# Performance work log

Hardware: AMD Instinct MI355X
Metric: run time of the kernel (lower is better)

Reference implementation:

```python
import jax, jax.numpy as jnp
import numpy as np

# Faithful translation of NeuralAggregation.forward (bias=False path):
#   proj = features @ W
#   out[n] = elementwise max over {0} union {a * proj[n] : a in adjacency[n]}
# Because proj[n] is fixed while a ranges over scalars,
#   max_k (a_k * proj[n,d]) == max(amax_n * proj[n,d], amin_n * proj[n,d])
# where amax_n / amin_n are the per-node max/min neighbor values. This avoids
# materializing the [N, deg, D] intermediate and is mathematically identical.

N_NODES = 100000
DEG = 32
DIM = 256


def setup_inputs() -> dict:
    key = jax.random.key(0)
    k1, k2, k3 = jax.random.split(key, 3)
    features = jax.random.normal(k1, (N_NODES, DIM), dtype=jnp.float32)
    adjacency = jax.random.uniform(k2, (N_NODES, DEG), dtype=jnp.float32)
    W = jax.random.normal(k3, (DIM, DIM), dtype=jnp.float32) * (1.0 / np.sqrt(DIM)).astype(np.float32)
    return {"features": features, "adjacency": adjacency, "W": W}


def reference(features, adjacency, W):
    proj = features @ W  # [N, D]
    amax = jnp.max(adjacency, axis=1, keepdims=True)  # [N, 1]
    amin = jnp.min(adjacency, axis=1, keepdims=True)  # [N, 1]
    agg = jnp.maximum(amax * proj, amin * proj)       # max over neighbors, elementwise
    return jnp.maximum(agg, 0.0)                      # torch.zeros init of `returning`
```

## Files before the change

kernel.cpp:

```cpp
#include <hip/hip_runtime.h>

#define N_NODES 100000
#define DEG 32
#define DIM 256

typedef _Float16 f16x8 __attribute__((ext_vector_type(8)));
typedef float f32x4 __attribute__((ext_vector_type(4)));

__global__ void wprep_kernel(const float* __restrict__ W, _Float16* __restrict__ Wswz) {
    int tid = blockIdx.x * blockDim.x + threadIdx.x;
    int l = tid & 63;
    int frag = tid >> 6;
    int kt = frag >> 4;
    int nt = frag & 15;
    int col = nt * 16 + (l & 15);
    int kbase = kt * 32 + ((l >> 4) << 2);
    f16x8 v;
#pragma unroll
    for (int j = 0; j < 8; ++j) {
        int k = kbase + (j & 3) + ((j >> 2) << 4);
        v[j] = (_Float16)W[(size_t)k * DIM + col];
    }
    *reinterpret_cast<f16x8*>(Wswz + (size_t)tid * 8) = v;
}

__device__ __forceinline__ f16x8 cvt_a(float4 lo, float4 hi) {
    f16x8 af;
    af[0] = (_Float16)lo.x; af[1] = (_Float16)lo.y;
    af[2] = (_Float16)lo.z; af[3] = (_Float16)lo.w;
    af[4] = (_Float16)hi.x; af[5] = (_Float16)hi.y;
    af[6] = (_Float16)hi.z; af[7] = (_Float16)hi.w;
    return af;
}

__launch_bounds__(256, 4)
__global__ void agg_kernel(const float* __restrict__ F, const float* __restrict__ Adj,
                           const _Float16* __restrict__ Wswz, float* __restrict__ out) {
    __shared__ _Float16 sB[32 * 64 * 8];

    const int bx = blockIdx.x;
    const int m0 = bx * 64;
    const int t  = threadIdx.x;
    const int wv = t >> 6;
    const int l  = t & 63;
    const int lg = l >> 4;
    const int ll = l & 15;

#pragma unroll
    for (int i = 0; i < 8; ++i) {
        int c = wv * 8 + i;
        int kt = c >> 2, np = c & 3;
        int srcfrag = kt * 16 + np;
        f16x8 v = *reinterpret_cast<const f16x8*>(Wswz + ((size_t)srcfrag * 64 + l) * 8);
        *reinterpret_cast<f16x8*>(&sB[((size_t)c * 64 + l) * 8]) = v;
    }

    const int rrow = t >> 2;
    const int q    = t & 3;
    int radj = m0 + rrow;
    radj = radj < N_NODES ? radj : (N_NODES - 1);
    const float4* ap = reinterpret_cast<const float4*>(Adj + (size_t)radj * DEG) + q * 2;
    float4 ad0 = ap[0], ad1 = ap[1];

    int rowA = m0 + wv * 16 + ll;
    rowA = rowA < N_NODES ? rowA : (N_NODES - 1);
    const float4* Af4 = reinterpret_cast<const float4*>(F + (size_t)rowA * DIM) + lg;
    float4 plo[8], phi[8];
#pragma unroll
    for (int kt = 0; kt < 8; ++kt) { plo[kt] = Af4[kt * 8]; phi[kt] = Af4[kt * 8 + 4]; }

    float mx = fmaxf(fmaxf(ad0.x, ad0.y), fmaxf(ad0.z, ad0.w));
    mx = fmaxf(mx, fmaxf(fmaxf(ad1.x, ad1.y), fmaxf(ad1.z, ad1.w)));
    float mn = fminf(fminf(ad0.x, ad0.y), fminf(ad0.z, ad0.w));
    mn = fminf(mn, fminf(fminf(ad1.x, ad1.y), fminf(ad1.z, ad1.w)));
    mx = fmaxf(mx, __shfl_xor(mx, 1)); mn = fminf(mn, __shfl_xor(mn, 1));
    mx = fmaxf(mx, __shfl_xor(mx, 2)); mn = fminf(mn, __shfl_xor(mn, 2));
    float amaxr[4], aminr[4];
#pragma unroll
    for (int r = 0; r < 4; ++r) {
        amaxr[r] = __shfl(mx, 16 * lg + 4 * r);
        aminr[r] = __shfl(mn, 16 * lg + 4 * r);
    }

    f16x8 a16[8];
#pragma unroll
    for (int kt = 0; kt < 8; ++kt) a16[kt] = cvt_a(plo[kt], phi[kt]);

    __syncthreads();

    const f16x8* Bl = reinterpret_cast<const f16x8*>(sB) + l;
    const int rbase = wv * 16 + 4 * lg;

#pragma unroll
    for (int p = 0; p < 4; ++p) {
        f32x4 acc[4];
#pragma unroll
        for (int np = 0; np < 4; ++np) acc[np] = (f32x4){0.f, 0.f, 0.f, 0.f};

#pragma unroll
        for (int kt = 0; kt < 8; ++kt) {
#pragma unroll
            for (int np = 0; np < 4; ++np) {
                f16x8 b = Bl[(kt * 4 + np) * 64];
                acc[np] = __builtin_amdgcn_mfma_f32_16x16x32_f16(a16[kt], b, acc[np], 0, 0, 0);
            }
        }
        __syncthreads();

        if (p < 3) {
#pragma unroll
            for (int i = 0; i < 8; ++i) {
                int c = wv * 8 + i;
                int kt = c >> 2, np = c & 3;
                int srcfrag = kt * 16 + (p + 1) * 4 + np;
                f16x8 v = *reinterpret_cast<const f16x8*>(Wswz + ((size_t)srcfrag * 64 + l) * 8);
                *reinterpret_cast<f16x8*>(&sB[((size_t)c * 64 + l) * 8]) = v;
            }
        }

#pragma unroll
        for (int r = 0; r < 4; ++r) {
            const int row = m0 + rbase + r;
            if (row < N_NODES) {
                float* orow = out + (size_t)row * DIM + p * 64 + ll;
#pragma unroll
                for (int np = 0; np < 4; ++np) {
                    float v = acc[np][r];
                    orow[np * 16] = fmaxf(fmaxf(amaxr[r] * v, aminr[r] * v), 0.0f);
                }
            }
        }

        if (p < 3) __syncthreads();
    }
}

extern "C" void kernel_launch(void* const* d_in, const int* in_sizes, int n_in,
                              void* d_out, int out_size, void* d_ws, size_t ws_size,
                              hipStream_t stream) {
    const float* F   = (const float*)d_in[0];
    const float* Adj = (const float*)d_in[1];
    const float* W   = (const float*)d_in[2];
    float* out = (float*)d_out;
    _Float16* Wswz = (_Float16*)d_ws;

    hipLaunchKernelGGL(wprep_kernel, dim3(32), dim3(256), 0, stream, W, Wswz);
    const int nblk = (N_NODES + 63) / 64;
    hipLaunchKernelGGL(agg_kernel, dim3(nblk), dim3(256), 0, stream, F, Adj, Wswz, out);
}
```

Measured before the change: 52.16 us.

## Retile waves as 2x2 over rows and columns to reuse B fragments

The kernel changes how each wave maps onto the 64x64 output sub-tile per pass. Each wave previously covered 16 rows by all 64 columns; it now covers 32 rows by 32 columns. Each B fragment read from LDS now feeds two MFMAs, which halves LDS reads per MFMA. The cost is that each wave loads and converts two rows' worth of A data (each feature row is now read by two waves), which raises register pressure under launch bounds of 4 blocks, and the adjacency min/max reduction is reorganised to match the new row mapping.

```diff
diff --git a/kernel.cpp b/kernel.cpp
--- a/kernel.cpp
+++ b/kernel.cpp
@@ -45,64 +45,83 @@
     const int l  = t & 63;
     const int lg = l >> 4;
     const int ll = l & 15;
+    const int mh = wv & 1;
+    const int nq = wv >> 1;
 
 #pragma unroll
     for (int i = 0; i < 8; ++i) {
         int c = wv * 8 + i;
-        int kt = c >> 2, np = c & 3;
-        int srcfrag = kt * 16 + np;
+        int kt = c >> 2, npp = c & 3;
+        int srcfrag = kt * 16 + npp;
         f16x8 v = *reinterpret_cast<const f16x8*>(Wswz + ((size_t)srcfrag * 64 + l) * 8);
         *reinterpret_cast<f16x8*>(&sB[((size_t)c * 64 + l) * 8]) = v;
     }
 
-    const int rrow = t >> 2;
-    const int q    = t & 3;
-    int radj = m0 + rrow;
+    const int arow = l >> 1;
+    const int q    = l & 1;
+    int radj = m0 + mh * 32 + arow;
     radj = radj < N_NODES ? radj : (N_NODES - 1);
-    const float4* ap = reinterpret_cast<const float4*>(Adj + (size_t)radj * DEG) + q * 2;
-    float4 ad0 = ap[0], ad1 = ap[1];
+    const float4* ap = reinterpret_cast<const float4*>(Adj + (size_t)radj * DEG) + q * 4;
+    float4 ad0 = ap[0], ad1 = ap[1], ad2 = ap[2], ad3 = ap[3];
 
-    int rowA = m0 + wv * 16 + ll;
-    rowA = rowA < N_NODES ? rowA : (N_NODES - 1);
-    const float4* Af4 = reinterpret_cast<const float4*>(F + (size_t)rowA * DIM) + lg;
+    int rowA0 = m0 + mh * 32 + ll;
+    rowA0 = rowA0 < N_NODES ? rowA0 : (N_NODES - 1);
+    const float4* Af0 = reinterpret_cast<const float4*>(F + (size_t)rowA0 * DIM) + lg;
     float4 plo[8], phi[8];
 #pragma unroll
-    for (int kt = 0; kt < 8; ++kt) { plo[kt] = Af4[kt * 8]; phi[kt] = Af4[kt * 8 + 4]; }
+    for (int kt = 0; kt < 8; ++kt) { plo[kt] = Af0[kt * 8]; phi[kt] = Af0[kt * 8 + 4]; }
 
     float mx = fmaxf(fmaxf(ad0.x, ad0.y), fmaxf(ad0.z, ad0.w));
     mx = fmaxf(mx, fmaxf(fmaxf(ad1.x, ad1.y), fmaxf(ad1.z, ad1.w)));
+    mx = fmaxf(mx, fmaxf(fmaxf(ad2.x, ad2.y), fmaxf(ad2.z, ad2.w)));
+    mx = fmaxf(mx, fmaxf(fmaxf(ad3.x, ad3.y), fmaxf(ad3.z, ad3.w)));
     float mn = fminf(fminf(ad0.x, ad0.y), fminf(ad0.z, ad0.w));
     mn = fminf(mn, fminf(fminf(ad1.x, ad1.y), fminf(ad1.z, ad1.w)));
-    mx = fmaxf(mx, __shfl_xor(mx, 1)); mn = fminf(mn, __shfl_xor(mn, 1));
-    mx = fmaxf(mx, __shfl_xor(mx, 2)); mn = fminf(mn, __shfl_xor(mn, 2));
-    float amaxr[4], aminr[4];
+    mn = fminf(mn, fminf(fminf(ad2.x, ad2.y), fminf(ad2.z, ad2.w)));
+    mn = fminf(mn, fminf(fminf(ad3.x, ad3.y), fminf(ad3.z, ad3.w)));
+    mx = fmaxf(mx, __shfl_xor(mx, 1));
+    mn = fminf(mn, __shfl_xor(mn, 1));
+    float amaxr[2][4], aminr[2][4];
 #pragma unroll
-    for (int r = 0; r < 4; ++r) {
-        amaxr[r] = __shfl(mx, 16 * lg + 4 * r);
-        aminr[r] = __shfl(mn, 16 * lg + 4 * r);
-    }
+    for (int s = 0; s < 2; ++s)
+#pragma unroll
+        for (int r = 0; r < 4; ++r) {
+            amaxr[s][r] = __shfl(mx, 2 * (s * 16 + 4 * lg + r));
+            aminr[s][r] = __shfl(mn, 2 * (s * 16 + 4 * lg + r));
+        }
 
-    f16x8 a16[8];
+    f16x8 a16[2][8];
 #pragma unroll
-    for (int kt = 0; kt < 8; ++kt) a16[kt] = cvt_a(plo[kt], phi[kt]);
+    for (int kt = 0; kt < 8; ++kt) a16[0][kt] = cvt_a(plo[kt], phi[kt]);
+
+    int rowA1 = m0 + mh * 32 + 16 + ll;
+    rowA1 = rowA1 < N_NODES ? rowA1 : (N_NODES - 1);
+    const float4* Af1 = reinterpret_cast<const float4*>(F + (size_t)rowA1 * DIM) + lg;
+#pragma unroll
+    for (int kt = 0; kt < 8; ++kt) { plo[kt] = Af1[kt * 8]; phi[kt] = Af1[kt * 8 + 4]; }
+#pragma unroll
+    for (int kt = 0; kt < 8; ++kt) a16[1][kt] = cvt_a(plo[kt], phi[kt]);
 
     __syncthreads();
 
     const f16x8* Bl = reinterpret_cast<const f16x8*>(sB) + l;
-    const int rbase = wv * 16 + 4 * lg;
+    const int rbase = 4 * lg;
 
 #pragma unroll
     for (int p = 0; p < 4; ++p) {
-        f32x4 acc[4];
+        f32x4 acc[2][2];
 #pragma unroll
-        for (int np = 0; np < 4; ++np) acc[np] = (f32x4){0.f, 0.f, 0.f, 0.f};
+        for (int s = 0; s < 2; ++s)
+#pragma unroll
+            for (int np = 0; np < 2; ++np) acc[s][np] = (f32x4){0.f, 0.f, 0.f, 0.f};
 
 #pragma unroll
         for (int kt = 0; kt < 8; ++kt) {
 #pragma unroll
-            for (int np = 0; np < 4; ++np) {
-                f16x8 b = Bl[(kt * 4 + np) * 64];
-                acc[np] = __builtin_amdgcn_mfma_f32_16x16x32_f16(a16[kt], b, acc[np], 0, 0, 0);
+            for (int np = 0; np < 2; ++np) {
+                f16x8 b = Bl[(kt * 4 + nq * 2 + np) * 64];
+                acc[0][np] = __builtin_amdgcn_mfma_f32_16x16x32_f16(a16[0][kt], b, acc[0][np], 0, 0, 0);
+                acc[1][np] = __builtin_amdgcn_mfma_f32_16x16x32_f16(a16[1][kt], b, acc[1][np], 0, 0, 0);
             }
         }
         __syncthreads();
@@ -111,25 +130,27 @@
 #pragma unroll
             for (int i = 0; i < 8; ++i) {
                 int c = wv * 8 + i;
-                int kt = c >> 2, np = c & 3;
-                int srcfrag = kt * 16 + (p + 1) * 4 + np;
+                int kt = c >> 2, npp = c & 3;
+                int srcfrag = kt * 16 + (p + 1) * 4 + npp;
                 f16x8 v = *reinterpret_cast<const f16x8*>(Wswz + ((size_t)srcfrag * 64 + l) * 8);
                 *reinterpret_cast<f16x8*>(&sB[((size_t)c * 64 + l) * 8]) = v;
             }
         }
 
 #pragma unroll
-        for (int r = 0; r < 4; ++r) {
-            const int row = m0 + rbase + r;
-            if (row < N_NODES) {
-                float* orow = out + (size_t)row * DIM + p * 64 + ll;
+        for (int s = 0; s < 2; ++s)
 #pragma unroll
-                for (int np = 0; np < 4; ++np) {
-                    float v = acc[np][r];
-                    orow[np * 16] = fmaxf(fmaxf(amaxr[r] * v, aminr[r] * v), 0.0f);
+            for (int r = 0; r < 4; ++r) {
+                const int row = m0 + mh * 32 + s * 16 + rbase + r;
+                if (row < N_NODES) {
+                    float* orow = out + (size_t)row * DIM + p * 64 + nq * 32 + ll;
+#pragma unroll
+                    for (int np = 0; np < 2; ++np) {
+                        float v = acc[s][np][r];
+                        orow[np * 16] = fmaxf(fmaxf(amaxr[s][r] * v, aminr[s][r] * v), 0.0f);
+                    }
                 }
             }
-        }
 
         if (p < 3) __syncthreads();
     }
```

After: 81.10 us. +55.5%, slower.
